# Kernel tuning notes

Hardware: AMD Instinct MI355X
Metric: run time of the kernel (lower is better)

Reference implementation:

```python
import jax, jax.numpy as jnp
import numpy as np


def setup_inputs() -> dict:
    key = jax.random.key(0)
    ks = jax.random.split(key, 5)
    N, C, W, H = 16, 256, 32, 32
    scale = 1.0 / np.sqrt(C)
    return {
        "x": jax.random.normal(ks[0], (N, C, W, H), dtype=jnp.float32),
        "w_theta": jax.random.normal(ks[1], (C, C), dtype=jnp.float32) * scale,
        "w_phi": jax.random.normal(ks[2], (C, C), dtype=jnp.float32) * scale,
        "w_g": jax.random.normal(ks[3], (C, C), dtype=jnp.float32) * scale,
        "w_restore": jax.random.normal(ks[4], (C, C), dtype=jnp.float32) * scale,
    }


def reference(x, w_theta, w_phi, w_g, w_restore):
    N, C, W, H = x.shape
    L = W * H
    xf = x.reshape(N, C, L)  # [N, C, L]
    # 1x1 convs == channel-mixing matmuls
    t = jnp.einsum('ac,ncl->nal', w_theta, xf)  # theta(x), [N, A, L]
    p = jnp.einsum('ac,ncl->nal', w_phi, xf)    # phi(x),   [N, A, L]
    g = jnp.einsum('ac,ncl->nal', w_g, xf)      # g(x),     [N, A, L]
    # c = x1 @ x2 with x1 = theta(x)^T : [N, L, L]
    c = jnp.einsum('nai,naj->nij', t, p)
    # GLOBAL softmax over the entire flattened L*L map per sample (not per-row)
    a = jax.nn.softmax(c.reshape(N, L * L), axis=1).reshape(N, L, L)
    # attn = g(x) @ a : [N, A, L] -> [N, A, W, H]
    attn = jnp.einsum('nai,nij->naj', g, a).reshape(N, C, W, H)
    # restore 1x1 conv back to in_features
    attn = jnp.einsum('ca,nawh->ncwh', w_restore, attn)
    return (c, x + attn)
```

## Files before the change

### kernel.cpp

```cpp
#include <hip/hip_runtime.h>
#include <hip/hip_bf16.h>

#define N_ 16
#define C_ 256
#define L_ 1024
#define LL_ (L_ * L_)
#define M0 128.0f

using bf16 = __hip_bfloat16;
typedef __bf16 bf16x8 __attribute__((ext_vector_type(8)));
typedef float f32x4 __attribute__((ext_vector_type(4)));

__device__ __forceinline__ float b2f(bf16 v) { return __bfloat162float(v); }
__device__ __forceinline__ bf16 f2b(float v) { return __float2bfloat16(v); }

__device__ __forceinline__ void glds16(const bf16* g, bf16* l) {
    __builtin_amdgcn_global_load_lds(
        (const __attribute__((address_space(1))) void*)g,
        (__attribute__((address_space(3))) void*)l, 16, 0, 0);
}

__device__ __forceinline__ unsigned packb2(float a, float b) {
    union { bf16 h; unsigned short u; } ua, ub;
    ua.h = f2b(a); ub.h = f2b(b);
    return (unsigned)ua.u | ((unsigned)ub.u << 16);
}

__device__ __forceinline__ float waveRedSum(float v) {
#pragma unroll
    for (int o = 32; o > 0; o >>= 1) v += __shfl_down(v, o, 64);
    return v;
}

__global__ void __launch_bounds__(256) k_prep(const float* __restrict__ wt,
                                              const float* __restrict__ wp,
                                              const float* __restrict__ wg,
                                              const float* __restrict__ wr,
                                              const float* __restrict__ x,
                                              bf16* __restrict__ Wstack,
                                              bf16* __restrict__ xT,
                                              float* __restrict__ sumv) {
    __shared__ unsigned sh[128 * 65];
    int b = blockIdx.x, t = threadIdx.x;
    if (b < 768) {
        if (b < 512) {
            int i = b * 256 + t;
            const float* src = (b < 256 ? wt : wp);
            Wstack[i] = f2b(src[i & 65535]);
        } else {
            int row = b - 512;
            const float* wrr = wr + row * 256;
            float acc = 0.f;
#pragma unroll 8
            for (int k = 0; k < 256; ++k) acc += wrr[k] * wg[k * 256 + t];
            Wstack[(size_t)b * 256 + t] = f2b(acc);
        }
        if (b == 0 && t < N_) sumv[t] = 0.f;
        return;
    }
    int bb = b - 768;
    int c0 = (bb & 7) * 128;
    int r0 = ((bb >> 3) & 1) * 128;
    int n = bb >> 4;
    const float* sp = x + (size_t)n * C_ * L_;
#pragma unroll
    for (int pass = 0; pass < 16; ++pass) {
        int idx = pass * 256 + t;
        int row = idx >> 5, cf4 = idx & 31;
        float4 v = *reinterpret_cast<const float4*>(
            sp + (size_t)(r0 + row) * L_ + c0 + cf4 * 4);
        sh[row * 65 + cf4 * 2]     = packb2(v.x, v.y);
        sh[row * 65 + cf4 * 2 + 1] = packb2(v.z, v.w);
    }
    __syncthreads();
    bf16* dp = xT + (size_t)n * L_ * C_;
#pragma unroll
    for (int pass = 0; pass < 8; ++pass) {
        int idx = pass * 256 + t;
        int ig = (idx & 3) + 4 * (idx >> 9);
        int jl = (idx >> 2) & 127;
        unsigned ow[4];
#pragma unroll
        for (int dpair = 0; dpair < 4; ++dpair) {
            int il = ig * 8 + dpair * 2;
            unsigned w0 = sh[il * 65 + (jl >> 1)];
            unsigned w1 = sh[(il + 1) * 65 + (jl >> 1)];
            unsigned a = (jl & 1) ? (w0 >> 16) : (w0 & 0xffffu);
            unsigned bv = (jl & 1) ? (w1 >> 16) : (w1 & 0xffffu);
            ow[dpair] = a | (bv << 16);
        }
        uint4 o; o.x = ow[0]; o.y = ow[1]; o.z = ow[2]; o.w = ow[3];
        *reinterpret_cast<uint4*>(dp + (size_t)(c0 + jl) * C_ + r0 + ig * 8) = o;
    }
}

__global__ void __launch_bounds__(256) k_tpg(const bf16* __restrict__ Wstack,
                                             const bf16* __restrict__ xT,
                                             bf16* __restrict__ tT, bf16* __restrict__ pT,
                                             bf16* __restrict__ gW) {
    __shared__ __align__(16) bf16 As[128 * 32];
    __shared__ __align__(16) bf16 Bs[128 * 32];
    const int t = threadIdx.x;
    const int lane = t & 63, wid = t >> 6;
    const int wr = wid >> 1, wc = wid & 1;
    const int q = lane >> 4, ln = lane & 15;
    const int l0 = blockIdx.x * 128, mt = blockIdx.y, n = blockIdx.z;
    const bf16* Ab = Wstack + (size_t)mt * 128 * C_;
    const bf16* Bb = xT + ((size_t)n * L_ + l0) * C_;
    const int sr = t >> 2, sk = (t & 3) * 8;
    bf16* AsW0 = &As[(size_t)(wid * 64) * 8];
    bf16* AsW1 = &As[(size_t)(wid * 64 + 256) * 8];
    bf16* BsW0 = &Bs[(size_t)(wid * 64) * 8];
    bf16* BsW1 = &Bs[(size_t)(wid * 64 + 256) * 8];

    f32x4 acc[4][4] = {};
    for (int kb = 0; kb < C_; kb += 32) {
        glds16(Ab + (size_t)sr * C_ + kb + sk, AsW0);
        glds16(Ab + (size_t)(sr + 64) * C_ + kb + sk, AsW1);
        glds16(Bb + (size_t)sr * C_ + kb + sk, BsW0);
        glds16(Bb + (size_t)(sr + 64) * C_ + kb + sk, BsW1);
        __syncthreads();
        bf16x8 af[4], bfr[4];
#pragma unroll
        for (int mi = 0; mi < 4; ++mi)
            af[mi] = *reinterpret_cast<const bf16x8*>(&As[(wr * 64 + mi * 16 + ln) * 32 + q * 8]);
#pragma unroll
        for (int ni = 0; ni < 4; ++ni)
            bfr[ni] = *reinterpret_cast<const bf16x8*>(&Bs[(wc * 64 + ni * 16 + ln) * 32 + q * 8]);
#pragma unroll
        for (int mi = 0; mi < 4; ++mi)
#pragma unroll
            for (int ni = 0; ni < 4; ++ni)
                acc[mi][ni] = __builtin_amdgcn_mfma_f32_16x16x32_bf16(af[mi], bfr[ni], acc[mi][ni], 0, 0, 0);
        __syncthreads();
    }
    int kind = mt >> 1;
    int mbase = (mt & 1) * 128;
    if (kind == 2) {
        bf16* ob = gW + (size_t)n * C_ * L_;
#pragma unroll
        for (int mi = 0; mi < 4; ++mi) {
            int a = mbase + wr * 64 + mi * 16 + q * 4;
#pragma unroll
            for (int ni = 0; ni < 4; ++ni) {
                int l = l0 + wc * 64 + ni * 16 + ln;
#pragma unroll
                for (int r = 0; r < 4; ++r)
                    ob[(size_t)(a + r) * L_ + l] = f2b(acc[mi][ni][r]);
            }
        }
    } else {
        bf16* ob = (kind == 0 ? tT : pT) + (size_t)n * L_ * C_;
#pragma unroll
        for (int mi = 0; mi < 4; ++mi) {
            int a = mbase + wr * 64 + mi * 16 + q * 4;
#pragma unroll
            for (int ni = 0; ni < 4; ++ni) {
                int l = l0 + wc * 64 + ni * 16 + ln;
                bf16 tmp[4];
#pragma unroll
                for (int r = 0; r < 4; ++r) tmp[r] = f2b(acc[mi][ni][r]);
                *reinterpret_cast<uint2*>(ob + (size_t)l * C_ + a) =
                    *reinterpret_cast<const uint2*>(tmp);
            }
        }
    }
}

__global__ void __launch_bounds__(256) k_cmat(const bf16* __restrict__ tT,
                                              const bf16* __restrict__ pT,
                                              float* __restrict__ cout,
                                              bf16* __restrict__ eT,
                                              float* __restrict__ sumv) {
    __shared__ __align__(16) bf16 As[128 * 32];
    __shared__ __align__(16) bf16 Bs[128 * 32];
    const int t = threadIdx.x;
    const int lane = t & 63, wid = t >> 6;
    const int wr = wid >> 1, wc = wid & 1;
    const int q = lane >> 4, ln = lane & 15;
    const int j0 = blockIdx.x * 128, i0 = blockIdx.y * 128, n = blockIdx.z;
    const bf16* Ab = tT + ((size_t)n * L_ + i0) * C_;
    const bf16* Bb = pT + ((size_t)n * L_ + j0) * C_;
    const int sr = t >> 2, sk = (t & 3) * 8;
    bf16* AsW0 = &As[(size_t)(wid * 64) * 8];
    bf16* AsW1 = &As[(size_t)(wid * 64 + 256) * 8];
    bf16* BsW0 = &Bs[(size_t)(wid * 64) * 8];
    bf16* BsW1 = &Bs[(size_t)(wid * 64 + 256) * 8];

    f32x4 acc[4][4] = {};
    for (int kb = 0; kb < C_; kb += 32) {
        glds16(Ab + (size_t)sr * C_ + kb + sk, AsW0);
        glds16(Ab + (size_t)(sr + 64) * C_ + kb + sk, AsW1);
        glds16(Bb + (size_t)sr * C_ + kb + sk, BsW0);
        glds16(Bb + (size_t)(sr + 64) * C_ + kb + sk, BsW1);
        __syncthreads();
        bf16x8 af[4], bfr[4];
#pragma unroll
        for (int mi = 0; mi < 4; ++mi)
            af[mi] = *reinterpret_cast<const bf16x8*>(&As[(wr * 64 + mi * 16 + ln) * 32 + q * 8]);
#pragma unroll
        for (int ni = 0; ni < 4; ++ni)
            bfr[ni] = *reinterpret_cast<const bf16x8*>(&Bs[(wc * 64 + ni * 16 + ln) * 32 + q * 8]);
#pragma unroll
        for (int mi = 0; mi < 4; ++mi)
#pragma unroll
            for (int ni = 0; ni < 4; ++ni)
                acc[mi][ni] = __builtin_amdgcn_mfma_f32_16x16x32_bf16(af[mi], bfr[ni], acc[mi][ni], 0, 0, 0);
        __syncthreads();
    }
    float s = 0.f;
    float* cb = cout + (size_t)n * LL_;
    bf16*  ep = eT + (size_t)n * LL_;
#pragma unroll
    for (int mi = 0; mi < 4; ++mi) {
        int i = i0 + wr * 64 + mi * 16 + q * 4;
#pragma unroll
        for (int ni = 0; ni < 4; ++ni) {
            int j = j0 + wc * 64 + ni * 16 + ln;
            bf16 tmp[4];
#pragma unroll
            for (int r = 0; r < 4; ++r) {
                float v = acc[mi][ni][r];
                cb[(size_t)(i + r) * L_ + j] = v;
                float e = __expf(v - M0);
                s += e;
                tmp[r] = f2b(e);
            }
            *reinterpret_cast<uint2*>(ep + (size_t)j * L_ + i) =
                *reinterpret_cast<const uint2*>(tmp);
        }
    }
    __shared__ float sh[4];
    s = waveRedSum(s);
    if (lane == 0) sh[wid] = s;
    __syncthreads();
    if (t == 0) atomicAdd(&sumv[n], sh[0] + sh[1] + sh[2] + sh[3]);
}

__global__ void __launch_bounds__(256) k_out(const bf16* __restrict__ gW,
                                             const bf16* __restrict__ eT,
                                             const float* __restrict__ sumv,
                                             const float* __restrict__ x,
                                             float* __restrict__ out) {
    __shared__ __align__(16) bf16 As[2][128 * 32];
    __shared__ __align__(16) bf16 Bs[2][128 * 32];
    const int t = threadIdx.x;
    const int lane = t & 63, wid = t >> 6;
    const int wr = wid >> 1, wc = wid & 1;
    const int q = lane >> 4, ln = lane & 15;
    const int j0 = blockIdx.x * 128, c0 = blockIdx.y * 128, n = blockIdx.z;
    const bf16* Ab = gW + ((size_t)n * C_ + c0) * L_;
    const bf16* Bb = eT + ((size_t)n * L_ + j0) * L_;
    const int sr = t >> 2, sk = (t & 3) * 8;
    const int w0 = (wid * 64) * 8, w1 = (wid * 64 + 256) * 8;

    auto stage = [&](int kb, int buf) {
        glds16(Ab + (size_t)sr * L_ + kb + sk, &As[buf][w0]);
        glds16(Ab + (size_t)(sr + 64) * L_ + kb + sk, &As[buf][w1]);
        glds16(Bb + (size_t)sr * L_ + kb + sk, &Bs[buf][w0]);
        glds16(Bb + (size_t)(sr + 64) * L_ + kb + sk, &Bs[buf][w1]);
    };

    f32x4 acc[4][4] = {};
    stage(0, 0);
    __syncthreads();
    int cur = 0;
    for (int kb = 0; kb < L_; kb += 32) {
        if (kb + 32 < L_) stage(kb + 32, cur ^ 1);
        bf16x8 af[4], bfr[4];
#pragma unroll
        for (int mi = 0; mi < 4; ++mi)
            af[mi] = *reinterpret_cast<const bf16x8*>(&As[cur][(wr * 64 + mi * 16 + ln) * 32 + q * 8]);
#pragma unroll
        for (int ni = 0; ni < 4; ++ni)
            bfr[ni] = *reinterpret_cast<const bf16x8*>(&Bs[cur][(wc * 64 + ni * 16 + ln) * 32 + q * 8]);
#pragma unroll
        for (int mi = 0; mi < 4; ++mi)
#pragma unroll
            for (int ni = 0; ni < 4; ++ni)
                acc[mi][ni] = __builtin_amdgcn_mfma_f32_16x16x32_bf16(af[mi], bfr[ni], acc[mi][ni], 0, 0, 0);
        __syncthreads();
        cur ^= 1;
    }
    float inv = 1.0f / sumv[n];
    const float* xb = x + (size_t)n * C_ * L_;
    float* ob = out + (size_t)n * C_ * L_;
#pragma unroll
    for (int mi = 0; mi < 4; ++mi) {
        int c = c0 + wr * 64 + mi * 16 + q * 4;
#pragma unroll
        for (int ni = 0; ni < 4; ++ni) {
            int j = j0 + wc * 64 + ni * 16 + ln;
#pragma unroll
            for (int r = 0; r < 4; ++r) {
                size_t off = (size_t)(c + r) * L_ + j;
                ob[off] = acc[mi][ni][r] * inv + xb[off];
            }
        }
    }
}

extern "C" void kernel_launch(void* const* d_in, const int* in_sizes, int n_in,
                              void* d_out, int out_size, void* d_ws, size_t ws_size,
                              hipStream_t stream) {
    const float* x  = (const float*)d_in[0];
    const float* wt = (const float*)d_in[1];
    const float* wp = (const float*)d_in[2];
    const float* wg = (const float*)d_in[3];
    const float* wr = (const float*)d_in[4];

    float* out_c = (float*)d_out;
    float* out_y = out_c + (size_t)N_ * LL_;

    bf16* tTb = (bf16*)out_y;
    bf16* pTb = tTb + (size_t)N_ * L_ * C_;

    char* base = (char*)d_ws;
    float* sumv   = (float*)base;
    bf16*  Wstack = (bf16*)(base + 1024);
    bf16*  xTb    = Wstack + 768 * 256;
    bf16*  gWb    = xTb + (size_t)N_ * L_ * C_;
    bf16*  eTb    = gWb + (size_t)N_ * C_ * L_;

    k_prep<<<dim3(1024), dim3(256), 0, stream>>>(wt, wp, wg, wr, x, Wstack, xTb, sumv);
    k_tpg<<<dim3(8, 6, 16), dim3(256), 0, stream>>>(Wstack, xTb, tTb, pTb, gWb);
    k_cmat<<<dim3(8, 8, 16), dim3(256), 0, stream>>>(tTb, pTb, out_c, eTb, sumv);
    k_out<<<dim3(8, 2, 16), dim3(256), 0, stream>>>(gWb, eTb, sumv, x, out_y);
}
```

Baseline: 181.1 us.

## Fuse projection, score and output GEMMs into one persistent kernel with grid barriers

Merges the three GEMM kernels into a single persistent kernel of 512 blocks that loops over tiles and separates the phases with atomic-counter grid barriers. This removes two launch gaps and tail-drain bubbles between stages. It also switches the large c and output stores to nontemporal stores. The output stage has only 256 tiles, so half the grid idles there. The spin barrier depends on all 512 blocks being co-resident and relies on a timeout guard to avoid deadlock.

Result: slower. 373.1 us (+106.1%).

```diff
diff --git a/kernel.cpp b/kernel.cpp
--- a/kernel.cpp
+++ b/kernel.cpp
@@ -5,13 +5,13 @@
 #define C_ 256
 #define L_ 1024
 #define LL_ (L_ * L_)
+#define GRID_ 512
 #define M0 128.0f
 
 using bf16 = __hip_bfloat16;
 typedef __bf16 bf16x8 __attribute__((ext_vector_type(8)));
 typedef float f32x4 __attribute__((ext_vector_type(4)));
 
-__device__ __forceinline__ float b2f(bf16 v) { return __bfloat162float(v); }
 __device__ __forceinline__ bf16 f2b(float v) { return __float2bfloat16(v); }
 
 __device__ __forceinline__ void glds16(const bf16* g, bf16* l) {
@@ -30,6 +30,22 @@
 #pragma unroll
     for (int o = 32; o > 0; o >>= 1) v += __shfl_down(v, o, 64);
     return v;
+}
+
+__device__ __forceinline__ void gbar(unsigned* cnt, unsigned target) {
+    __syncthreads();
+    if (threadIdx.x == 0) {
+        __threadfence();
+        atomicAdd(cnt, 1u);
+        int guard = 0;
+        while (__hip_atomic_load(cnt, __ATOMIC_ACQUIRE,
+                                 __HIP_MEMORY_SCOPE_AGENT) < target) {
+            __builtin_amdgcn_s_sleep(8);
+            if (++guard > (1 << 20)) break;
+        }
+        __threadfence();
+    }
+    __syncthreads();
 }
 
 __global__ void __launch_bounds__(256) k_prep(const float* __restrict__ wt,
@@ -39,7 +55,8 @@
                                               const float* __restrict__ x,
                                               bf16* __restrict__ Wstack,
                                               bf16* __restrict__ xT,
-                                              float* __restrict__ sumv) {
+                                              float* __restrict__ sumv,
+                                              unsigned* __restrict__ bar) {
     __shared__ unsigned sh[128 * 65];
     int b = blockIdx.x, t = threadIdx.x;
     if (b < 768) {
@@ -55,13 +72,14 @@
             for (int k = 0; k < 256; ++k) acc += wrr[k] * wg[k * 256 + t];
             Wstack[(size_t)b * 256 + t] = f2b(acc);
         }
-        if (b == 0 && t < N_) sumv[t] = 0.f;
+        if (b == 0) {
+            if (t < N_) sumv[t] = 0.f;
+            if (t >= 32 && t < 36) bar[t - 32] = 0u;
+        }
         return;
     }
     int bb = b - 768;
-    int c0 = (bb & 7) * 128;
-    int r0 = ((bb >> 3) & 1) * 128;
-    int n = bb >> 4;
+    int c0 = (bb & 7) * 128, r0 = ((bb >> 3) & 1) * 128, n = bb >> 4;
     const float* sp = x + (size_t)n * C_ * L_;
 #pragma unroll
     for (int pass = 0; pass < 16; ++pass) {
@@ -81,221 +99,213 @@
         int jl = (idx >> 2) & 127;
         unsigned ow[4];
 #pragma unroll
-        for (int dpair = 0; dpair < 4; ++dpair) {
-            int il = ig * 8 + dpair * 2;
+        for (int dp2 = 0; dp2 < 4; ++dp2) {
+            int il = ig * 8 + dp2 * 2;
             unsigned w0 = sh[il * 65 + (jl >> 1)];
             unsigned w1 = sh[(il + 1) * 65 + (jl >> 1)];
             unsigned a = (jl & 1) ? (w0 >> 16) : (w0 & 0xffffu);
             unsigned bv = (jl & 1) ? (w1 >> 16) : (w1 & 0xffffu);
-            ow[dpair] = a | (bv << 16);
+            ow[dp2] = a | (bv << 16);
         }
         uint4 o; o.x = ow[0]; o.y = ow[1]; o.z = ow[2]; o.w = ow[3];
         *reinterpret_cast<uint4*>(dp + (size_t)(c0 + jl) * C_ + r0 + ig * 8) = o;
     }
 }
 
-__global__ void __launch_bounds__(256) k_tpg(const bf16* __restrict__ Wstack,
-                                             const bf16* __restrict__ xT,
-                                             bf16* __restrict__ tT, bf16* __restrict__ pT,
-                                             bf16* __restrict__ gW) {
-    __shared__ __align__(16) bf16 As[128 * 32];
-    __shared__ __align__(16) bf16 Bs[128 * 32];
+__global__ void __launch_bounds__(256, 2) k_fused(
+    const float* __restrict__ x,
+    const bf16* __restrict__ Wstack, const bf16* __restrict__ xT,
+    bf16* tT, bf16* pT,
+    bf16* __restrict__ gW, bf16* __restrict__ eT,
+    float* __restrict__ sumv, unsigned* __restrict__ bar,
+    float* __restrict__ cout,
+    float* out) {
+    __shared__ __align__(16) bf16 smem[16384];
+    __shared__ float sred[4];
+
+    const int bid = blockIdx.x;
     const int t = threadIdx.x;
     const int lane = t & 63, wid = t >> 6;
-    const int wr = wid >> 1, wc = wid & 1;
+    const int wr_ = wid >> 1, wc_ = wid & 1;
     const int q = lane >> 4, ln = lane & 15;
-    const int l0 = blockIdx.x * 128, mt = blockIdx.y, n = blockIdx.z;
-    const bf16* Ab = Wstack + (size_t)mt * 128 * C_;
-    const bf16* Bb = xT + ((size_t)n * L_ + l0) * C_;
     const int sr = t >> 2, sk = (t & 3) * 8;
-    bf16* AsW0 = &As[(size_t)(wid * 64) * 8];
-    bf16* AsW1 = &As[(size_t)(wid * 64 + 256) * 8];
-    bf16* BsW0 = &Bs[(size_t)(wid * 64) * 8];
-    bf16* BsW1 = &Bs[(size_t)(wid * 64 + 256) * 8];
-
-    f32x4 acc[4][4] = {};
-    for (int kb = 0; kb < C_; kb += 32) {
-        glds16(Ab + (size_t)sr * C_ + kb + sk, AsW0);
-        glds16(Ab + (size_t)(sr + 64) * C_ + kb + sk, AsW1);
-        glds16(Bb + (size_t)sr * C_ + kb + sk, BsW0);
-        glds16(Bb + (size_t)(sr + 64) * C_ + kb + sk, BsW1);
+
+    bf16* AsP = smem;
+    bf16* BsP = smem + 4096;
+    bf16* AsW0 = &AsP[(wid * 64) * 8];
+    bf16* AsW1 = &AsP[(wid * 64 + 256) * 8];
+    bf16* BsW0 = &BsP[(wid * 64) * 8];
+    bf16* BsW1 = &BsP[(wid * 64 + 256) * 8];
+
+    for (int u = bid; u < 768; u += GRID_) {
+        int l0 = (u & 7) * 128;
+        int rem = u >> 3;
+        int mt = rem % 6, n = rem / 6;
+        const bf16* Ab = Wstack + (size_t)mt * 128 * C_;
+        const bf16* Bb = xT + ((size_t)n * L_ + l0) * C_;
+        f32x4 acc[4][4] = {};
+        for (int kb = 0; kb < C_; kb += 32) {
+            glds16(Ab + (size_t)sr * C_ + kb + sk, AsW0);
+            glds16(Ab + (size_t)(sr + 64) * C_ + kb + sk, AsW1);
+            glds16(Bb + (size_t)sr * C_ + kb + sk, BsW0);
+            glds16(Bb + (size_t)(sr + 64) * C_ + kb + sk, BsW1);
+            __syncthreads();
+            bf16x8 af[4], bfr[4];
+#pragma unroll
+            for (int mi = 0; mi < 4; ++mi)
+                af[mi] = *reinterpret_cast<const bf16x8*>(&AsP[(wr_ * 64 + mi * 16 + ln) * 32 + q * 8]);
+#pragma unroll
+            for (int ni = 0; ni < 4; ++ni)
+                bfr[ni] = *reinterpret_cast<const bf16x8*>(&BsP[(wc_ * 64 + ni * 16 + ln) * 32 + q * 8]);
+#pragma unroll
+            for (int mi = 0; mi < 4; ++mi)
+#pragma unroll
+                for (int ni = 0; ni < 4; ++ni)
+                    acc[mi][ni] = __builtin_amdgcn_mfma_f32_16x16x32_bf16(af[mi], bfr[ni], acc[mi][ni], 0, 0, 0);
+            __syncthreads();
+        }
+        int kind = mt >> 1;
+        int mbase = (mt & 1) * 128;
+        if (kind == 2) {
+            bf16* ob = gW + (size_t)n * C_ * L_;
+#pragma unroll
+            for (int mi = 0; mi < 4; ++mi) {
+                int a = mbase + wr_ * 64 + mi * 16 + q * 4;
+#pragma unroll
+                for (int ni = 0; ni < 4; ++ni) {
+                    int l = l0 + wc_ * 64 + ni * 16 + ln;
+#pragma unroll
+                    for (int r = 0; r < 4; ++r)
+                        ob[(size_t)(a + r) * L_ + l] = f2b(acc[mi][ni][r]);
+                }
+            }
+        } else {
+            bf16* ob = (kind == 0 ? tT : pT) + (size_t)n * L_ * C_;
+#pragma unroll
+            for (int mi = 0; mi < 4; ++mi) {
+                int a = mbase + wr_ * 64 + mi * 16 + q * 4;
+#pragma unroll
+                for (int ni = 0; ni < 4; ++ni) {
+                    int l = l0 + wc_ * 64 + ni * 16 + ln;
+                    bf16 tmp[4];
+#pragma unroll
+                    for (int r = 0; r < 4; ++r) tmp[r] = f2b(acc[mi][ni][r]);
+                    *reinterpret_cast<uint2*>(ob + (size_t)l * C_ + a) =
+                        *reinterpret_cast<const uint2*>(tmp);
+                }
+            }
+        }
+    }
+    gbar(&bar[0], GRID_);
+
+    for (int u = bid; u < 1024; u += GRID_) {
+        int j0 = (u & 7) * 128, i0 = ((u >> 3) & 7) * 128, n = u >> 6;
+        const bf16* Ab = tT + ((size_t)n * L_ + i0) * C_;
+        const bf16* Bb = pT + ((size_t)n * L_ + j0) * C_;
+        f32x4 acc[4][4] = {};
+        for (int kb = 0; kb < C_; kb += 32) {
+            glds16(Ab + (size_t)sr * C_ + kb + sk, AsW0);
+            glds16(Ab + (size_t)(sr + 64) * C_ + kb + sk, AsW1);
+            glds16(Bb + (size_t)sr * C_ + kb + sk, BsW0);
+            glds16(Bb + (size_t)(sr + 64) * C_ + kb + sk, BsW1);
+            __syncthreads();
+            bf16x8 af[4], bfr[4];
+#pragma unroll
+            for (int mi = 0; mi < 4; ++mi)
+                af[mi] = *reinterpret_cast<const bf16x8*>(&AsP[(wr_ * 64 + mi * 16 + ln) * 32 + q * 8]);
+#pragma unroll
+            for (int ni = 0; ni < 4; ++ni)
+                bfr[ni] = *reinterpret_cast<const bf16x8*>(&BsP[(wc_ * 64 + ni * 16 + ln) * 32 + q * 8]);
+#pragma unroll
+            for (int mi = 0; mi < 4; ++mi)
+#pragma unroll
+                for (int ni = 0; ni < 4; ++ni)
+                    acc[mi][ni] = __builtin_amdgcn_mfma_f32_16x16x32_bf16(af[mi], bfr[ni], acc[mi][ni], 0, 0, 0);
+            __syncthreads();
+        }
+        float s = 0.f;
+        float* cb = cout + (size_t)n * LL_;
+        bf16*  ep = eT + (size_t)n * LL_;
+#pragma unroll
+        for (int mi = 0; mi < 4; ++mi) {
+            int i = i0 + wr_ * 64 + mi * 16 + q * 4;
+#pragma unroll
+            for (int ni = 0; ni < 4; ++ni) {
+                int j = j0 + wc_ * 64 + ni * 16 + ln;
+                bf16 tmp[4];
+#pragma unroll
+                for (int r = 0; r < 4; ++r) {
+                    float v = acc[mi][ni][r];
+                    __builtin_nontemporal_store(v, &cb[(size_t)(i + r) * L_ + j]);
+                    float e = __expf(v - M0);
+                    s += e;
+                    tmp[r] = f2b(e);
+                }
+                *reinterpret_cast<uint2*>(ep + (size_t)j * L_ + i) =
+                    *reinterpret_cast<const uint2*>(tmp);
+            }
+        }
+        s = waveRedSum(s);
+        if (lane == 0) sred[wid] = s;
         __syncthreads();
-        bf16x8 af[4], bfr[4];
-#pragma unroll
-        for (int mi = 0; mi < 4; ++mi)
-            af[mi] = *reinterpret_cast<const bf16x8*>(&As[(wr * 64 + mi * 16 + ln) * 32 + q * 8]);
-#pragma unroll
-        for (int ni = 0; ni < 4; ++ni)
-            bfr[ni] = *reinterpret_cast<const bf16x8*>(&Bs[(wc * 64 + ni * 16 + ln) * 32 + q * 8]);
-#pragma unroll
-        for (int mi = 0; mi < 4; ++mi)
-#pragma unroll
-            for (int ni = 0; ni < 4; ++ni)
-                acc[mi][ni] = __builtin_amdgcn_mfma_f32_16x16x32_bf16(af[mi], bfr[ni], acc[mi][ni], 0, 0, 0);
+        if (t == 0) atomicAdd(&sumv[n], sred[0] + sred[1] + sred[2] + sred[3]);
         __syncthreads();
     }
-    int kind = mt >> 1;
-    int mbase = (mt & 1) * 128;
-    if (kind == 2) {
-        bf16* ob = gW + (size_t)n * C_ * L_;
-#pragma unroll
-        for (int mi = 0; mi < 4; ++mi) {
-            int a = mbase + wr * 64 + mi * 16 + q * 4;
-#pragma unroll
-            for (int ni = 0; ni < 4; ++ni) {
-                int l = l0 + wc * 64 + ni * 16 + ln;
-#pragma unroll
-                for (int r = 0; r < 4; ++r)
-                    ob[(size_t)(a + r) * L_ + l] = f2b(acc[mi][ni][r]);
-            }
-        }
-    } else {
-        bf16* ob = (kind == 0 ? tT : pT) + (size_t)n * L_ * C_;
-#pragma unroll
-        for (int mi = 0; mi < 4; ++mi) {
-            int a = mbase + wr * 64 + mi * 16 + q * 4;
-#pragma unroll
-            for (int ni = 0; ni < 4; ++ni) {
-                int l = l0 + wc * 64 + ni * 16 + ln;
-                bf16 tmp[4];
-#pragma unroll
-                for (int r = 0; r < 4; ++r) tmp[r] = f2b(acc[mi][ni][r]);
-                *reinterpret_cast<uint2*>(ob + (size_t)l * C_ + a) =
-                    *reinterpret_cast<const uint2*>(tmp);
-            }
-        }
-    }
-}
-
-__global__ void __launch_bounds__(256) k_cmat(const bf16* __restrict__ tT,
-                                              const bf16* __restrict__ pT,
-                                              float* __restrict__ cout,
-                                              bf16* __restrict__ eT,
-                                              float* __restrict__ sumv) {
-    __shared__ __align__(16) bf16 As[128 * 32];
-    __shared__ __align__(16) bf16 Bs[128 * 32];
-    const int t = threadIdx.x;
-    const int lane = t & 63, wid = t >> 6;
-    const int wr = wid >> 1, wc = wid & 1;
-    const int q = lane >> 4, ln = lane & 15;
-    const int j0 = blockIdx.x * 128, i0 = blockIdx.y * 128, n = blockIdx.z;
-    const bf16* Ab = tT + ((size_t)n * L_ + i0) * C_;
-    const bf16* Bb = pT + ((size_t)n * L_ + j0) * C_;
-    const int sr = t >> 2, sk = (t & 3) * 8;
-    bf16* AsW0 = &As[(size_t)(wid * 64) * 8];
-    bf16* AsW1 = &As[(size_t)(wid * 64 + 256) * 8];
-    bf16* BsW0 = &Bs[(size_t)(wid * 64) * 8];
-    bf16* BsW1 = &Bs[(size_t)(wid * 64 + 256) * 8];
-
-    f32x4 acc[4][4] = {};
-    for (int kb = 0; kb < C_; kb += 32) {
-        glds16(Ab + (size_t)sr * C_ + kb + sk, AsW0);
-        glds16(Ab + (size_t)(sr + 64) * C_ + kb + sk, AsW1);
-        glds16(Bb + (size_t)sr * C_ + kb + sk, BsW0);
-        glds16(Bb + (size_t)(sr + 64) * C_ + kb + sk, BsW1);
-        __syncthreads();
-        bf16x8 af[4], bfr[4];
-#pragma unroll
-        for (int mi = 0; mi < 4; ++mi)
-            af[mi] = *reinterpret_cast<const bf16x8*>(&As[(wr * 64 + mi * 16 + ln) * 32 + q * 8]);
-#pragma unroll
-        for (int ni = 0; ni < 4; ++ni)
-            bfr[ni] = *reinterpret_cast<const bf16x8*>(&Bs[(wc * 64 + ni * 16 + ln) * 32 + q * 8]);
-#pragma unroll
-        for (int mi = 0; mi < 4; ++mi)
-#pragma unroll
-            for (int ni = 0; ni < 4; ++ni)
-                acc[mi][ni] = __builtin_amdgcn_mfma_f32_16x16x32_bf16(af[mi], bfr[ni], acc[mi][ni], 0, 0, 0);
-        __syncthreads();
-    }
-    float s = 0.f;
-    float* cb = cout + (size_t)n * LL_;
-    bf16*  ep = eT + (size_t)n * LL_;
-#pragma unroll
-    for (int mi = 0; mi < 4; ++mi) {
-        int i = i0 + wr * 64 + mi * 16 + q * 4;
-#pragma unroll
-        for (int ni = 0; ni < 4; ++ni) {
-            int j = j0 + wc * 64 + ni * 16 + ln;
-            bf16 tmp[4];
-#pragma unroll
-            for (int r = 0; r < 4; ++r) {
-                float v = acc[mi][ni][r];
-                cb[(size_t)(i + r) * L_ + j] = v;
-                float e = __expf(v - M0);
-                s += e;
-                tmp[r] = f2b(e);
-            }
-            *reinterpret_cast<uint2*>(ep + (size_t)j * L_ + i) =
-                *reinterpret_cast<const uint2*>(tmp);
-        }
-    }
-    __shared__ float sh[4];
-    s = waveRedSum(s);
-    if (lane == 0) sh[wid] = s;
-    __syncthreads();
-    if (t == 0) atomicAdd(&sumv[n], sh[0] + sh[1] + sh[2] + sh[3]);
-}
-
-__global__ void __launch_bounds__(256) k_out(const bf16* __restrict__ gW,
-                                             const bf16* __restrict__ eT,
-                                             const float* __restrict__ sumv,
-                                             const float* __restrict__ x,
-                                             float* __restrict__ out) {
-    __shared__ __align__(16) bf16 As[2][128 * 32];
-    __shared__ __align__(16) bf16 Bs[2][128 * 32];
-    const int t = threadIdx.x;
-    const int lane = t & 63, wid = t >> 6;
-    const int wr = wid >> 1, wc = wid & 1;
-    const int q = lane >> 4, ln = lane & 15;
-    const int j0 = blockIdx.x * 128, c0 = blockIdx.y * 128, n = blockIdx.z;
-    const bf16* Ab = gW + ((size_t)n * C_ + c0) * L_;
-    const bf16* Bb = eT + ((size_t)n * L_ + j0) * L_;
-    const int sr = t >> 2, sk = (t & 3) * 8;
-    const int w0 = (wid * 64) * 8, w1 = (wid * 64 + 256) * 8;
-
-    auto stage = [&](int kb, int buf) {
-        glds16(Ab + (size_t)sr * L_ + kb + sk, &As[buf][w0]);
-        glds16(Ab + (size_t)(sr + 64) * L_ + kb + sk, &As[buf][w1]);
-        glds16(Bb + (size_t)sr * L_ + kb + sk, &Bs[buf][w0]);
-        glds16(Bb + (size_t)(sr + 64) * L_ + kb + sk, &Bs[buf][w1]);
-    };
-
-    f32x4 acc[4][4] = {};
-    stage(0, 0);
-    __syncthreads();
-    int cur = 0;
-    for (int kb = 0; kb < L_; kb += 32) {
-        if (kb + 32 < L_) stage(kb + 32, cur ^ 1);
-        bf16x8 af[4], bfr[4];
-#pragma unroll
-        for (int mi = 0; mi < 4; ++mi)
-            af[mi] = *reinterpret_cast<const bf16x8*>(&As[cur][(wr * 64 + mi * 16 + ln) * 32 + q * 8]);
-#pragma unroll
-        for (int ni = 0; ni < 4; ++ni)
-            bfr[ni] = *reinterpret_cast<const bf16x8*>(&Bs[cur][(wc * 64 + ni * 16 + ln) * 32 + q * 8]);
-#pragma unroll
-        for (int mi = 0; mi < 4; ++mi)
-#pragma unroll
-            for (int ni = 0; ni < 4; ++ni)
-                acc[mi][ni] = __builtin_amdgcn_mfma_f32_16x16x32_bf16(af[mi], bfr[ni], acc[mi][ni], 0, 0, 0);
-        __syncthreads();
-        cur ^= 1;
-    }
-    float inv = 1.0f / sumv[n];
-    const float* xb = x + (size_t)n * C_ * L_;
-    float* ob = out + (size_t)n * C_ * L_;
-#pragma unroll
-    for (int mi = 0; mi < 4; ++mi) {
-        int c = c0 + wr * 64 + mi * 16 + q * 4;
-#pragma unroll
-        for (int ni = 0; ni < 4; ++ni) {
-            int j = j0 + wc * 64 + ni * 16 + ln;
-#pragma unroll
-            for (int r = 0; r < 4; ++r) {
-                size_t off = (size_t)(c + r) * L_ + j;
-                ob[off] = acc[mi][ni][r] * inv + xb[off];
-            }
+    gbar(&bar[1], GRID_);
+
+    {
+        bf16* As2 = smem;
+        bf16* Bs2 = smem + 8192;
+        const int w0 = (wid * 64) * 8, w1 = (wid * 64 + 256) * 8;
+        for (int u = bid; u < 256; u += GRID_) {
+            int j0 = (u & 7) * 128, c0 = ((u >> 3) & 1) * 128, n = u >> 4;
+            const bf16* Ab = gW + ((size_t)n * C_ + c0) * L_;
+            const bf16* Bb = eT + ((size_t)n * L_ + j0) * L_;
+            auto stage = [&](int kb, int buf) {
+                glds16(Ab + (size_t)sr * L_ + kb + sk, As2 + buf * 4096 + w0);
+                glds16(Ab + (size_t)(sr + 64) * L_ + kb + sk, As2 + buf * 4096 + w1);
+                glds16(Bb + (size_t)sr * L_ + kb + sk, Bs2 + buf * 4096 + w0);
+                glds16(Bb + (size_t)(sr + 64) * L_ + kb + sk, Bs2 + buf * 4096 + w1);
+            };
+            f32x4 acc[4][4] = {};
+            stage(0, 0);
+            __syncthreads();
+            int cur = 0;
+            for (int kb = 0; kb < L_; kb += 32) {
+                if (kb + 32 < L_) stage(kb + 32, cur ^ 1);
+                bf16x8 af[4], bfr[4];
+#pragma unroll
+                for (int mi = 0; mi < 4; ++mi)
+                    af[mi] = *reinterpret_cast<const bf16x8*>(&As2[cur * 4096 + (wr_ * 64 + mi * 16 + ln) * 32 + q * 8]);
+#pragma unroll
+                for (int ni = 0; ni < 4; ++ni)
+                    bfr[ni] = *reinterpret_cast<const bf16x8*>(&Bs2[cur * 4096 + (wc_ * 64 + ni * 16 + ln) * 32 + q * 8]);
+#pragma unroll
+                for (int mi = 0; mi < 4; ++mi)
+#pragma unroll
+                    for (int ni = 0; ni < 4; ++ni)
+                        acc[mi][ni] = __builtin_amdgcn_mfma_f32_16x16x32_bf16(af[mi], bfr[ni], acc[mi][ni], 0, 0, 0);
+                __syncthreads();
+                cur ^= 1;
+            }
+            float inv = 1.0f / sumv[n];
+            const float* xb = x + (size_t)n * C_ * L_;
+            float* ob = out + (size_t)n * C_ * L_;
+#pragma unroll
+            for (int mi = 0; mi < 4; ++mi) {
+                int c = c0 + wr_ * 64 + mi * 16 + q * 4;
+#pragma unroll
+                for (int ni = 0; ni < 4; ++ni) {
+                    int j = j0 + wc_ * 64 + ni * 16 + ln;
+#pragma unroll
+                    for (int r = 0; r < 4; ++r) {
+                        size_t off = (size_t)(c + r) * L_ + j;
+                        __builtin_nontemporal_store(
+                            acc[mi][ni][r] * inv + xb[off], &ob[off]);
+                    }
+                }
+            }
+            __syncthreads();
         }
     }
 }
@@ -316,14 +326,16 @@
     bf16* pTb = tTb + (size_t)N_ * L_ * C_;
 
     char* base = (char*)d_ws;
-    float* sumv   = (float*)base;
-    bf16*  Wstack = (bf16*)(base + 1024);
-    bf16*  xTb    = Wstack + 768 * 256;
-    bf16*  gWb    = xTb + (size_t)N_ * L_ * C_;
-    bf16*  eTb    = gWb + (size_t)N_ * C_ * L_;
-
-    k_prep<<<dim3(1024), dim3(256), 0, stream>>>(wt, wp, wg, wr, x, Wstack, xTb, sumv);
-    k_tpg<<<dim3(8, 6, 16), dim3(256), 0, stream>>>(Wstack, xTb, tTb, pTb, gWb);
-    k_cmat<<<dim3(8, 8, 16), dim3(256), 0, stream>>>(tTb, pTb, out_c, eTb, sumv);
-    k_out<<<dim3(8, 2, 16), dim3(256), 0, stream>>>(gWb, eTb, sumv, x, out_y);
-}
+    float*    sumv   = (float*)base;
+    unsigned* bar    = (unsigned*)(base + 128);
+    bf16*     Wstack = (bf16*)(base + 1024);
+    bf16*     xTb    = Wstack + 768 * 256;
+    bf16*     gWb    = xTb + (size_t)N_ * L_ * C_;
+    bf16*     eTb    = gWb + (size_t)N_ * C_ * L_;
+
+    k_prep<<<dim3(1024), dim3(256), 0, stream>>>(wt, wp, wg, wr, x,
+                                                 Wstack, xTb, sumv, bar);
+    k_fused<<<dim3(GRID_), dim3(256), 0, stream>>>(x, Wstack, xTb, tTb, pTb,
+                                                   gWb, eTb, sumv, bar,
+                                                   out_c, out_y);
+}
```

## Stage transposed exp tile through swizzled LDS and halve k_out tile width

Applied to the files above, without the earlier changes.

In k_cmat, the transposed bf16 exp tile is now written into a swizzled shared-memory buffer first and then stored to global memory as coalesced 16-byte rows. Before, each thread wrote scattered 8-byte chunks. In k_out, the N tile shrinks from 128 to 64 columns and the grid doubles to 512 blocks, which should fill more CUs on the device. The trade-off is that each k_out block now reuses A data across fewer columns, and k_cmat gains an extra barrier and LDS round trip.

Result: faster. 174.2 us (median of 3 runs) (-3.8%).

```diff
diff --git a/kernel.cpp b/kernel.cpp
--- a/kernel.cpp
+++ b/kernel.cpp
@@ -11,7 +11,6 @@
 typedef __bf16 bf16x8 __attribute__((ext_vector_type(8)));
 typedef float f32x4 __attribute__((ext_vector_type(4)));
 
-__device__ __forceinline__ float b2f(bf16 v) { return __bfloat162float(v); }
 __device__ __forceinline__ bf16 f2b(float v) { return __float2bfloat16(v); }
 
 __device__ __forceinline__ void glds16(const bf16* g, bf16* l) {
@@ -59,9 +58,7 @@
         return;
     }
     int bb = b - 768;
-    int c0 = (bb & 7) * 128;
-    int r0 = ((bb >> 3) & 1) * 128;
-    int n = bb >> 4;
+    int c0 = (bb & 7) * 128, r0 = ((bb >> 3) & 1) * 128, n = bb >> 4;
     const float* sp = x + (size_t)n * C_ * L_;
 #pragma unroll
     for (int pass = 0; pass < 16; ++pass) {
@@ -81,13 +78,13 @@
         int jl = (idx >> 2) & 127;
         unsigned ow[4];
 #pragma unroll
-        for (int dpair = 0; dpair < 4; ++dpair) {
-            int il = ig * 8 + dpair * 2;
+        for (int dp2 = 0; dp2 < 4; ++dp2) {
+            int il = ig * 8 + dp2 * 2;
             unsigned w0 = sh[il * 65 + (jl >> 1)];
             unsigned w1 = sh[(il + 1) * 65 + (jl >> 1)];
             unsigned a = (jl & 1) ? (w0 >> 16) : (w0 & 0xffffu);
             unsigned bv = (jl & 1) ? (w1 >> 16) : (w1 & 0xffffu);
-            ow[dpair] = a | (bv << 16);
+            ow[dp2] = a | (bv << 16);
         }
         uint4 o; o.x = ow[0]; o.y = ow[1]; o.z = ow[2]; o.w = ow[3];
         *reinterpret_cast<uint4*>(dp + (size_t)(c0 + jl) * C_ + r0 + ig * 8) = o;
@@ -108,10 +105,10 @@
     const bf16* Ab = Wstack + (size_t)mt * 128 * C_;
     const bf16* Bb = xT + ((size_t)n * L_ + l0) * C_;
     const int sr = t >> 2, sk = (t & 3) * 8;
-    bf16* AsW0 = &As[(size_t)(wid * 64) * 8];
-    bf16* AsW1 = &As[(size_t)(wid * 64 + 256) * 8];
-    bf16* BsW0 = &Bs[(size_t)(wid * 64) * 8];
-    bf16* BsW1 = &Bs[(size_t)(wid * 64 + 256) * 8];
+    bf16* AsW0 = &As[(wid * 64) * 8];
+    bf16* AsW1 = &As[(wid * 64 + 256) * 8];
+    bf16* BsW0 = &Bs[(wid * 64) * 8];
+    bf16* BsW1 = &Bs[(wid * 64 + 256) * 8];
 
     f32x4 acc[4][4] = {};
     for (int kb = 0; kb < C_; kb += 32) {
@@ -172,8 +169,10 @@
                                               float* __restrict__ cout,
                                               bf16* __restrict__ eT,
                                               float* __restrict__ sumv) {
-    __shared__ __align__(16) bf16 As[128 * 32];
-    __shared__ __align__(16) bf16 Bs[128 * 32];
+    __shared__ __align__(16) bf16 smem[16384];
+    __shared__ float sred[4];
+    bf16* AsP = smem;
+    bf16* BsP = smem + 4096;
     const int t = threadIdx.x;
     const int lane = t & 63, wid = t >> 6;
     const int wr = wid >> 1, wc = wid & 1;
@@ -182,10 +181,10 @@
     const bf16* Ab = tT + ((size_t)n * L_ + i0) * C_;
     const bf16* Bb = pT + ((size_t)n * L_ + j0) * C_;
     const int sr = t >> 2, sk = (t & 3) * 8;
-    bf16* AsW0 = &As[(size_t)(wid * 64) * 8];
-    bf16* AsW1 = &As[(size_t)(wid * 64 + 256) * 8];
-    bf16* BsW0 = &Bs[(size_t)(wid * 64) * 8];
-    bf16* BsW1 = &Bs[(size_t)(wid * 64 + 256) * 8];
+    bf16* AsW0 = &AsP[(wid * 64) * 8];
+    bf16* AsW1 = &AsP[(wid * 64 + 256) * 8];
+    bf16* BsW0 = &BsP[(wid * 64) * 8];
+    bf16* BsW1 = &BsP[(wid * 64 + 256) * 8];
 
     f32x4 acc[4][4] = {};
     for (int kb = 0; kb < C_; kb += 32) {
@@ -197,10 +196,10 @@
         bf16x8 af[4], bfr[4];
 #pragma unroll
         for (int mi = 0; mi < 4; ++mi)
-            af[mi] = *reinterpret_cast<const bf16x8*>(&As[(wr * 64 + mi * 16 + ln) * 32 + q * 8]);
+            af[mi] = *reinterpret_cast<const bf16x8*>(&AsP[(wr * 64 + mi * 16 + ln) * 32 + q * 8]);
 #pragma unroll
         for (int ni = 0; ni < 4; ++ni)
-            bfr[ni] = *reinterpret_cast<const bf16x8*>(&Bs[(wc * 64 + ni * 16 + ln) * 32 + q * 8]);
+            bfr[ni] = *reinterpret_cast<const bf16x8*>(&BsP[(wc * 64 + ni * 16 + ln) * 32 + q * 8]);
 #pragma unroll
         for (int mi = 0; mi < 4; ++mi)
 #pragma unroll
@@ -210,31 +209,40 @@
     }
     float s = 0.f;
     float* cb = cout + (size_t)n * LL_;
-    bf16*  ep = eT + (size_t)n * LL_;
+    char* esh = (char*)smem;
 #pragma unroll
     for (int mi = 0; mi < 4; ++mi) {
-        int i = i0 + wr * 64 + mi * 16 + q * 4;
+        int il = wr * 64 + mi * 16 + q * 4;
 #pragma unroll
         for (int ni = 0; ni < 4; ++ni) {
-            int j = j0 + wc * 64 + ni * 16 + ln;
+            int jl = wc * 64 + ni * 16 + ln;
             bf16 tmp[4];
 #pragma unroll
             for (int r = 0; r < 4; ++r) {
                 float v = acc[mi][ni][r];
-                cb[(size_t)(i + r) * L_ + j] = v;
+                cb[(size_t)(i0 + il + r) * L_ + (j0 + jl)] = v;
                 float e = __expf(v - M0);
                 s += e;
                 tmp[r] = f2b(e);
             }
-            *reinterpret_cast<uint2*>(ep + (size_t)j * L_ + i) =
+            unsigned boff = (unsigned)jl * 256 + (((unsigned)il * 2) ^ (((unsigned)jl & 7) << 4));
+            *reinterpret_cast<uint2*>(esh + boff) =
                 *reinterpret_cast<const uint2*>(tmp);
         }
     }
-    __shared__ float sh[4];
+    __syncthreads();
+    bf16* ep = eT + (size_t)n * LL_;
+#pragma unroll
+    for (int p = 0; p < 8; ++p) {
+        int j = p * 16 + (t >> 4), ch = t & 15;
+        unsigned roff = (unsigned)j * 256 + (((unsigned)ch * 16) ^ (((unsigned)j & 7) << 4));
+        uint4 v = *reinterpret_cast<const uint4*>(esh + roff);
+        *reinterpret_cast<uint4*>(ep + (size_t)(j0 + j) * L_ + i0 + ch * 8) = v;
+    }
     s = waveRedSum(s);
-    if (lane == 0) sh[wid] = s;
+    if (lane == 0) sred[wid] = s;
     __syncthreads();
-    if (t == 0) atomicAdd(&sumv[n], sh[0] + sh[1] + sh[2] + sh[3]);
+    if (t == 0) atomicAdd(&sumv[n], sred[0] + sred[1] + sred[2] + sred[3]);
 }
 
 __global__ void __launch_bounds__(256) k_out(const bf16* __restrict__ gW,
@@ -242,42 +250,40 @@
                                              const float* __restrict__ sumv,
                                              const float* __restrict__ x,
                                              float* __restrict__ out) {
-    __shared__ __align__(16) bf16 As[2][128 * 32];
-    __shared__ __align__(16) bf16 Bs[2][128 * 32];
+    __shared__ __align__(16) bf16 As2[2][4096];
+    __shared__ __align__(16) bf16 Bs2[2][2048];
     const int t = threadIdx.x;
     const int lane = t & 63, wid = t >> 6;
     const int wr = wid >> 1, wc = wid & 1;
     const int q = lane >> 4, ln = lane & 15;
-    const int j0 = blockIdx.x * 128, c0 = blockIdx.y * 128, n = blockIdx.z;
+    const int j0 = blockIdx.x * 64, c0 = blockIdx.y * 128, n = blockIdx.z;
     const bf16* Ab = gW + ((size_t)n * C_ + c0) * L_;
     const bf16* Bb = eT + ((size_t)n * L_ + j0) * L_;
     const int sr = t >> 2, sk = (t & 3) * 8;
-    const int w0 = (wid * 64) * 8, w1 = (wid * 64 + 256) * 8;
 
     auto stage = [&](int kb, int buf) {
-        glds16(Ab + (size_t)sr * L_ + kb + sk, &As[buf][w0]);
-        glds16(Ab + (size_t)(sr + 64) * L_ + kb + sk, &As[buf][w1]);
-        glds16(Bb + (size_t)sr * L_ + kb + sk, &Bs[buf][w0]);
-        glds16(Bb + (size_t)(sr + 64) * L_ + kb + sk, &Bs[buf][w1]);
+        glds16(Ab + (size_t)sr * L_ + kb + sk, &As2[buf][wid * 512]);
+        glds16(Ab + (size_t)(sr + 64) * L_ + kb + sk, &As2[buf][2048 + wid * 512]);
+        glds16(Bb + (size_t)sr * L_ + kb + sk, &Bs2[buf][wid * 512]);
     };
 
-    f32x4 acc[4][4] = {};
+    f32x4 acc[4][2] = {};
     stage(0, 0);
     __syncthreads();
     int cur = 0;
     for (int kb = 0; kb < L_; kb += 32) {
         if (kb + 32 < L_) stage(kb + 32, cur ^ 1);
-        bf16x8 af[4], bfr[4];
-#pragma unroll
-        for (int mi = 0; mi < 4; ++mi)
-            af[mi] = *reinterpret_cast<const bf16x8*>(&As[cur][(wr * 64 + mi * 16 + ln) * 32 + q * 8]);
-#pragma unroll
-        for (int ni = 0; ni < 4; ++ni)
-            bfr[ni] = *reinterpret_cast<const bf16x8*>(&Bs[cur][(wc * 64 + ni * 16 + ln) * 32 + q * 8]);
-#pragma unroll
-        for (int mi = 0; mi < 4; ++mi)
-#pragma unroll
-            for (int ni = 0; ni < 4; ++ni)
+        bf16x8 af[4], bfr[2];
+#pragma unroll
+        for (int mi = 0; mi < 4; ++mi)
+            af[mi] = *reinterpret_cast<const bf16x8*>(&As2[cur][(wr * 64 + mi * 16 + ln) * 32 + q * 8]);
+#pragma unroll
+        for (int ni = 0; ni < 2; ++ni)
+            bfr[ni] = *reinterpret_cast<const bf16x8*>(&Bs2[cur][(wc * 32 + ni * 16 + ln) * 32 + q * 8]);
+#pragma unroll
+        for (int mi = 0; mi < 4; ++mi)
+#pragma unroll
+            for (int ni = 0; ni < 2; ++ni)
                 acc[mi][ni] = __builtin_amdgcn_mfma_f32_16x16x32_bf16(af[mi], bfr[ni], acc[mi][ni], 0, 0, 0);
         __syncthreads();
         cur ^= 1;
@@ -289,8 +295,8 @@
     for (int mi = 0; mi < 4; ++mi) {
         int c = c0 + wr * 64 + mi * 16 + q * 4;
 #pragma unroll
-        for (int ni = 0; ni < 4; ++ni) {
-            int j = j0 + wc * 64 + ni * 16 + ln;
+        for (int ni = 0; ni < 2; ++ni) {
+            int j = j0 + wc * 32 + ni * 16 + ln;
 #pragma unroll
             for (int r = 0; r < 4; ++r) {
                 size_t off = (size_t)(c + r) * L_ + j;
@@ -325,5 +331,5 @@
     k_prep<<<dim3(1024), dim3(256), 0, stream>>>(wt, wp, wg, wr, x, Wstack, xTb, sumv);
     k_tpg<<<dim3(8, 6, 16), dim3(256), 0, stream>>>(Wstack, xTb, tTb, pTb, gWb);
     k_cmat<<<dim3(8, 8, 16), dim3(256), 0, stream>>>(tTb, pTb, out_c, eTb, sumv);
-    k_out<<<dim3(8, 2, 16), dim3(256), 0, stream>>>(gWb, eTb, sumv, x, out_y);
-}
+    k_out<<<dim3(16, 2, 16), dim3(256), 0, stream>>>(gWb, eTb, sumv, x, out_y);
+}
```
